# Performance work log

Hardware: AMD Instinct MI355X
Metric: run time of the kernel (lower is better)

The kernel has to match this reference:

```python
import jax, jax.numpy as jnp
import numpy as np

B, X_DIM, Z_DIM, K = 16384, 784, 64, 64
LOG2PI = 1.8378770664093453


def setup_inputs() -> dict:
    key = jax.random.key(0)
    ks = jax.random.split(key, 8)
    pi_raw = jax.random.uniform(ks[1], (B, K), dtype=jnp.float32) + 1e-3
    pi = pi_raw / jnp.sum(pi_raw, axis=1, keepdims=True)
    return {
        "x": jax.random.normal(ks[0], (B, X_DIM), dtype=jnp.float32),
        "pi": pi,
        "qz_mu": jax.random.normal(ks[2], (B, Z_DIM), dtype=jnp.float32),
        "qz_logsigma": 0.5 * jax.random.normal(ks[3], (B, Z_DIM), dtype=jnp.float32),
        "eps": jax.random.normal(ks[4], (B, Z_DIM), dtype=jnp.float32),
        "pz_y_mu": jax.random.normal(ks[5], (K, Z_DIM), dtype=jnp.float32),
        "pz_y_logsigma": jnp.zeros((K, Z_DIM), dtype=jnp.float32),  # log(init_sigma=1.0)
        "W_dec": jax.random.normal(ks[6], (Z_DIM, X_DIM), dtype=jnp.float32) / np.sqrt(Z_DIM),
        "b_dec": jnp.zeros((X_DIM,), dtype=jnp.float32),
    }


def reference(x, pi, qz_mu, qz_logsigma, eps, pz_y_mu, pz_y_logsigma, W_dec, b_dec):
    # GMMVAE.elbo with num_samples=1; rsample reparameterized with fixed eps.
    qs = jnp.exp(qz_logsigma)                      # [B, z]
    z = qz_mu + qs * eps                           # [B, z]

    # log p(x | z): unit-variance Gaussian likelihood with linear decoder
    mean = z @ W_dec + b_dec                       # [B, x]
    log_px_z = jnp.sum(-0.5 * (x - mean) ** 2 - 0.5 * LOG2PI)

    # py_z: vectorized over all k components (fuses the original Python loop)
    ps = jnp.exp(pz_y_logsigma)                    # [k, z]
    diff = z[:, None, :] - pz_y_mu[None, :, :]     # [B, k, z]
    comp_lp = jnp.sum(-0.5 * (diff / ps[None]) ** 2 - pz_y_logsigma[None] - 0.5 * LOG2PI, axis=-1)  # [B, k]
    log_pi = jnp.log(pi)
    pzy = comp_lp + log_pi                         # [B, k]
    log_py_z = pzy - jax.scipy.special.logsumexp(pzy, axis=1, keepdims=True)
    probs = jnp.exp(log_py_z)                      # [B, k]

    # kl_y = sum_b KL(Cat(py_z) || Cat(pi))
    kl_y = jnp.sum(probs * (log_py_z - log_pi))

    # kl_z = sum_b sum_k probs[b,k] * KL(N(qz_mu, qs) || N(mu_k, ps_k)).sum(z)
    mdiff = qz_mu[:, None, :] - pz_y_mu[None, :, :]  # [B, k, z]
    klz_bk = jnp.sum(
        pz_y_logsigma[None] - qz_logsigma[:, None, :]
        + (qs[:, None, :] ** 2 + mdiff ** 2) / (2.0 * ps[None] ** 2)
        - 0.5,
        axis=-1,
    )                                              # [B, k]
    kl_z = jnp.sum(probs * klz_bk)

    elbo = (log_px_z - kl_y - kl_z) / x.shape[0]
    return elbo
```

## Files before the change

### kernel.cpp

```cpp
#include <hip/hip_runtime.h>

#define NB 16384
#define XD 784
#define ZD 64
#define KK 64
#define LOG2PI_F 1.8378770664093453f
#define LDA 72

typedef __attribute__((ext_vector_type(8))) short short8;
typedef __attribute__((ext_vector_type(4))) float floatx4;


__device__ __forceinline__ float wave_sum(float x) {
    #pragma unroll
    for (int o = 32; o > 0; o >>= 1) x += __shfl_xor(x, o, 64);
    return x;
}

__device__ __forceinline__ unsigned short f2bf(float f) {
    unsigned u = __float_as_uint(f);
    unsigned r = (u + 0x7FFF + ((u >> 16) & 1)) >> 16;
    return (unsigned short)r;
}

__device__ __forceinline__ unsigned int pack2(float a, float b) {
    return (unsigned int)f2bf(a) | ((unsigned int)f2bf(b) << 16);
}

__global__ __launch_bounds__(256) void prep_kernel(
    const float* __restrict__ W, unsigned short* __restrict__ Wt)
{
    int idx = blockIdx.x * 256 + threadIdx.x;
    if (idx < ZD * XD) {
        int k = idx / XD;
        int n = idx - k * XD;
        Wt[n * ZD + k] = f2bf(W[idx]);
    }
}

__global__ __launch_bounds__(256) void mixture_mfma_kernel(
    const float* __restrict__ pi, const float* __restrict__ qmu,
    const float* __restrict__ qls, const float* __restrict__ eps,
    const float* __restrict__ pmu_g, const float* __restrict__ plog_g,
    float* __restrict__ kly_p, float* __restrict__ klz_p)
{
    __shared__ unsigned short Az2[64 * LDA];
    __shared__ unsigned short Azm[64 * LDA];
    __shared__ unsigned short Aq2[64 * LDA];
    __shared__ unsigned short Aqm[64 * LDA];
    __shared__ unsigned short Bi2[64 * LDA];
    __shared__ unsigned short Bm1[64 * LDA];
    __shared__ float Ck_s[KK], Sk_s[KK], Gk_s[KK], sq_s[64];
    __shared__ float r1[4], r2[4];

    const int tid  = threadIdx.x;
    const int row0 = blockIdx.x * 64;

    {
        const int r  = tid >> 2;
        const int q  = tid & 3;
        const int v0 = q * 16;
        const int gb = (row0 + r) * 64 + v0;
        float4 mu4[4], ls4[4], ep4[4];
        #pragma unroll
        for (int i = 0; i < 4; ++i) {
            mu4[i] = *(const float4*)&qmu[gb + 4 * i];
            ls4[i] = *(const float4*)&qls[gb + 4 * i];
            ep4[i] = *(const float4*)&eps[gb + 4 * i];
        }
        float sls = 0.f;
        unsigned int* pz2 = (unsigned int*)&Az2[r * LDA + v0];
        unsigned int* pzm = (unsigned int*)&Azm[r * LDA + v0];
        unsigned int* pq2 = (unsigned int*)&Aq2[r * LDA + v0];
        unsigned int* pqm = (unsigned int*)&Aqm[r * LDA + v0];
        #pragma unroll
        for (int i = 0; i < 4; ++i) {
            float m0[4] = {mu4[i].x, mu4[i].y, mu4[i].z, mu4[i].w};
            float l0[4] = {ls4[i].x, ls4[i].y, ls4[i].z, ls4[i].w};
            float e0[4] = {ep4[i].x, ep4[i].y, ep4[i].z, ep4[i].w};
            float z[4], q2[4];
            #pragma unroll
            for (int j = 0; j < 4; ++j) {
                float qs = __expf(l0[j]);
                z[j]  = fmaf(qs, e0[j], m0[j]);
                q2[j] = fmaf(m0[j], m0[j], qs * qs);
                sls += l0[j];
            }
            pz2[i * 2 + 0] = pack2(z[0] * z[0], z[1] * z[1]);
            pz2[i * 2 + 1] = pack2(z[2] * z[2], z[3] * z[3]);
            pzm[i * 2 + 0] = pack2(-2.f * z[0], -2.f * z[1]);
            pzm[i * 2 + 1] = pack2(-2.f * z[2], -2.f * z[3]);
            pq2[i * 2 + 0] = pack2(q2[0], q2[1]);
            pq2[i * 2 + 1] = pack2(q2[2], q2[3]);
            pqm[i * 2 + 0] = pack2(-2.f * m0[0], -2.f * m0[1]);
            pqm[i * 2 + 1] = pack2(-2.f * m0[2], -2.f * m0[3]);
        }
        sls += __shfl_xor(sls, 1, 64);
        sls += __shfl_xor(sls, 2, 64);
        if (q == 0) sq_s[r] = sls;
    }

    {
        const int k  = tid >> 2;
        const int q  = tid & 3;
        const int v0 = q * 16;
        const int gb = k * 64 + v0;
        float s = 0.f, g = 0.f;
        unsigned int* pi2 = (unsigned int*)&Bi2[k * LDA + v0];
        unsigned int* pm1 = (unsigned int*)&Bm1[k * LDA + v0];
        #pragma unroll
        for (int i = 0; i < 4; ++i) {
            float4 mu4 = *(const float4*)&pmu_g[gb + 4 * i];
            float4 lg4 = *(const float4*)&plog_g[gb + 4 * i];
            float m0[4] = {mu4.x, mu4.y, mu4.z, mu4.w};
            float l0[4] = {lg4.x, lg4.y, lg4.z, lg4.w};
            float i2v[4], m1v[4];
            #pragma unroll
            for (int j = 0; j < 4; ++j) {
                float i2 = 0.5f * __expf(-2.f * l0[j]);
                i2v[j] = i2;
                m1v[j] = m0[j] * i2;
                g = fmaf(m0[j] * m0[j], i2, g);
                s += l0[j];
            }
            pi2[i * 2 + 0] = pack2(i2v[0], i2v[1]);
            pi2[i * 2 + 1] = pack2(i2v[2], i2v[3]);
            pm1[i * 2 + 0] = pack2(m1v[0], m1v[1]);
            pm1[i * 2 + 1] = pack2(m1v[2], m1v[3]);
        }
        s += __shfl_xor(s, 1, 64);
        s += __shfl_xor(s, 2, 64);
        g += __shfl_xor(g, 1, 64);
        g += __shfl_xor(g, 2, 64);
        if (q == 0) {
            Sk_s[k] = s;
            Gk_s[k] = g;
            Ck_s[k] = -s - 32.0f * LOG2PI_F;
        }
    }
    __syncthreads();

    const int lane  = tid & 63;
    const int wid   = tid >> 6;
    const int mm    = lane & 15;
    const int quad  = lane >> 4;
    const int rbase = wid * 16;

    const short8 az2_0 = *(const short8*)&Az2[(rbase + mm) * LDA + quad * 8];
    const short8 az2_1 = *(const short8*)&Az2[(rbase + mm) * LDA + 32 + quad * 8];
    const short8 azm_0 = *(const short8*)&Azm[(rbase + mm) * LDA + quad * 8];
    const short8 azm_1 = *(const short8*)&Azm[(rbase + mm) * LDA + 32 + quad * 8];
    const short8 aq2_0 = *(const short8*)&Aq2[(rbase + mm) * LDA + quad * 8];
    const short8 aq2_1 = *(const short8*)&Aq2[(rbase + mm) * LDA + 32 + quad * 8];
    const short8 aqm_0 = *(const short8*)&Aqm[(rbase + mm) * LDA + quad * 8];
    const short8 aqm_1 = *(const short8*)&Aqm[(rbase + mm) * LDA + 32 + quad * 8];

    floatx4 acc_a[4], acc_c[4];
    #pragma unroll
    for (int t = 0; t < 4; ++t) {
        const int kr = t * 16 + mm;
        const short8 bi0 = *(const short8*)&Bi2[kr * LDA + quad * 8];
        const short8 bi1 = *(const short8*)&Bi2[kr * LDA + 32 + quad * 8];
        const short8 bm0 = *(const short8*)&Bm1[kr * LDA + quad * 8];
        const short8 bm1 = *(const short8*)&Bm1[kr * LDA + 32 + quad * 8];
        floatx4 ca = {0.f, 0.f, 0.f, 0.f};
        ca = __builtin_amdgcn_mfma_f32_16x16x32_bf16(az2_0, bi0, ca, 0, 0, 0);
        ca = __builtin_amdgcn_mfma_f32_16x16x32_bf16(az2_1, bi1, ca, 0, 0, 0);
        ca = __builtin_amdgcn_mfma_f32_16x16x32_bf16(azm_0, bm0, ca, 0, 0, 0);
        ca = __builtin_amdgcn_mfma_f32_16x16x32_bf16(azm_1, bm1, ca, 0, 0, 0);
        acc_a[t] = ca;
        floatx4 cc = {0.f, 0.f, 0.f, 0.f};
        cc = __builtin_amdgcn_mfma_f32_16x16x32_bf16(aq2_0, bi0, cc, 0, 0, 0);
        cc = __builtin_amdgcn_mfma_f32_16x16x32_bf16(aq2_1, bi1, cc, 0, 0, 0);
        cc = __builtin_amdgcn_mfma_f32_16x16x32_bf16(aqm_0, bm0, cc, 0, 0, 0);
        cc = __builtin_amdgcn_mfma_f32_16x16x32_bf16(aqm_1, bm1, cc, 0, 0, 0);
        acc_c[t] = cc;
    }

    float comp[4][4], pz[4][4];
    #pragma unroll
    for (int t = 0; t < 4; ++t) {
        const int k = t * 16 + mm;
        const float ck = Ck_s[k], gk = Gk_s[k];
        #pragma unroll
        for (int r = 0; r < 4; ++r) {
            const int gb = row0 + rbase + quad * 4 + r;
            comp[t][r] = ck - (acc_a[t][r] + gk);
            pz[t][r] = comp[t][r] + __logf(pi[gb * 64 + k]);
        }
    }

    float kly = 0.f, klz = 0.f;
    #pragma unroll
    for (int r = 0; r < 4; ++r) {
        float mx = fmaxf(fmaxf(pz[0][r], pz[1][r]), fmaxf(pz[2][r], pz[3][r]));
        #pragma unroll
        for (int o = 1; o <= 8; o <<= 1) mx = fmaxf(mx, __shfl_xor(mx, o, 64));
        float e[4];
        float s = 0.f;
        #pragma unroll
        for (int t = 0; t < 4; ++t) { e[t] = __expf(pz[t][r] - mx); s += e[t]; }
        #pragma unroll
        for (int o = 1; o <= 8; o <<= 1) s += __shfl_xor(s, o, 64);
        const float lse = mx + __logf(s);
        const float inv = __frcp_rn(s);
        const float sql = sq_s[rbase + quad * 4 + r];
        #pragma unroll
        for (int t = 0; t < 4; ++t) {
            const int k = t * 16 + mm;
            const float p = e[t] * inv;
            kly = fmaf(p, comp[t][r] - lse, kly);
            const float cv = acc_c[t][r] + Gk_s[k];
            klz = fmaf(p, Sk_s[k] - sql + cv - 32.0f, klz);
        }
    }

    kly = wave_sum(kly);
    klz = wave_sum(klz);
    if (lane == 0) { r1[wid] = kly; r2[wid] = klz; }
    __syncthreads();
    if (tid == 0) {
        kly_p[blockIdx.x] = r1[0] + r1[1] + r1[2] + r1[3];
        klz_p[blockIdx.x] = r2[0] + r2[1] + r2[2] + r2[3];
    }
}

__global__ __launch_bounds__(256) void decoder_mfma_kernel(
    const float* __restrict__ x, const float* __restrict__ qmu,
    const float* __restrict__ qls, const float* __restrict__ eps,
    const unsigned short* __restrict__ Wt, const float* __restrict__ bd,
    float* __restrict__ dec_p)
{
    __shared__ unsigned short zt[16 * 64];
    __shared__ float rs[4];
    const int tid  = threadIdx.x;
    const int row0 = blockIdx.x * 16;

    for (int i = tid; i < 16 * 64; i += 256) {
        int g = row0 * 64 + i;
        float z = fmaf(__expf(qls[g]), eps[g], qmu[g]);
        zt[i] = f2bf(z);
    }
    __syncthreads();

    const int lane = tid & 63;
    const int wid  = tid >> 6;
    const int m    = lane & 15;
    const int quad = lane >> 4;

    const short8 af0 = *(const short8*)&zt[m * 64 + quad * 8];
    const short8 af1 = *(const short8*)&zt[m * 64 + 32 + quad * 8];

    const int xrow = (row0 + quad * 4) * XD;

    float xa0, xa1, xa2, xa3, bb;
    short8 w0, w1;
    {
        const int col = wid * 16 + m;
        xa0 = x[xrow + 0 * XD + col];
        xa1 = x[xrow + 1 * XD + col];
        xa2 = x[xrow + 2 * XD + col];
        xa3 = x[xrow + 3 * XD + col];
        bb  = bd[col];
        w0  = *(const short8*)&Wt[col * 64 + quad * 8];
        w1  = *(const short8*)&Wt[col * 64 + 32 + quad * 8];
    }

    float accl = 0.f;
    #pragma unroll 1
    for (int t = wid; t < 49; t += 4) {
        const float cx0 = xa0, cx1 = xa1, cx2 = xa2, cx3 = xa3, cb = bb;
        const short8 cw0 = w0, cw1 = w1;
        const int tn = t + 4;
        if (tn < 49) {
            const int col = tn * 16 + m;
            xa0 = x[xrow + 0 * XD + col];
            xa1 = x[xrow + 1 * XD + col];
            xa2 = x[xrow + 2 * XD + col];
            xa3 = x[xrow + 3 * XD + col];
            bb  = bd[col];
            w0  = *(const short8*)&Wt[col * 64 + quad * 8];
            w1  = *(const short8*)&Wt[col * 64 + 32 + quad * 8];
        }
        floatx4 c = {0.f, 0.f, 0.f, 0.f};
        c = __builtin_amdgcn_mfma_f32_16x16x32_bf16(af0, cw0, c, 0, 0, 0);
        c = __builtin_amdgcn_mfma_f32_16x16x32_bf16(af1, cw1, c, 0, 0, 0);
        float d0 = cx0 - (c[0] + cb);
        float d1 = cx1 - (c[1] + cb);
        float d2 = cx2 - (c[2] + cb);
        float d3 = cx3 - (c[3] + cb);
        accl = fmaf(d0, d0, accl);
        accl = fmaf(d1, d1, accl);
        accl = fmaf(d2, d2, accl);
        accl = fmaf(d3, d3, accl);
    }

    float s = wave_sum(accl);
    if (lane == 0) rs[wid] = s;
    __syncthreads();
    if (tid == 0)
        dec_p[blockIdx.x] = -0.5f * (rs[0] + rs[1] + rs[2] + rs[3]);
}

__global__ __launch_bounds__(256) void finalize_kernel(
    const float* __restrict__ dec_p, const float* __restrict__ kly_p,
    const float* __restrict__ klz_p, float* __restrict__ out)
{
    __shared__ double s0[256], s1[256], s2[256];
    const int tid = threadIdx.x;
    double a0 = 0.0, a1 = 0.0, a2 = 0.0;
    for (int i = tid; i < 1024; i += 256) a0 += (double)dec_p[i];
    a1 = (double)kly_p[tid];
    a2 = (double)klz_p[tid];
    s0[tid] = a0; s1[tid] = a1; s2[tid] = a2;
    __syncthreads();
    #pragma unroll
    for (int off = 128; off > 0; off >>= 1) {
        if (tid < off) {
            s0[tid] += s0[tid + off];
            s1[tid] += s1[tid + off];
            s2[tid] += s2[tid + off];
        }
        __syncthreads();
    }
    if (tid == 0) {
        double lpx = s0[0] - 0.5 * 1.8378770664093453 * (double)NB * (double)XD;
        out[0] = (float)((lpx - s1[0] - s2[0]) / (double)NB);
    }
}

extern "C" void kernel_launch(void* const* d_in, const int* in_sizes, int n_in,
                              void* d_out, int out_size, void* d_ws, size_t ws_size,
                              hipStream_t stream) {
    const float* x    = (const float*)d_in[0];
    const float* pi   = (const float*)d_in[1];
    const float* qmu  = (const float*)d_in[2];
    const float* qls  = (const float*)d_in[3];
    const float* eps  = (const float*)d_in[4];
    const float* pmu  = (const float*)d_in[5];
    const float* plog = (const float*)d_in[6];
    const float* W    = (const float*)d_in[7];
    const float* bd   = (const float*)d_in[8];
    float* out = (float*)d_out;

    unsigned short* Wt = (unsigned short*)d_ws;
    float* fp    = (float*)((char*)d_ws + 100352);
    float* dec_p = fp;
    float* kly_p = fp + 1024;
    float* klz_p = fp + 1280;

    prep_kernel<<<(ZD * XD + 255) / 256, 256, 0, stream>>>(W, Wt);
    mixture_mfma_kernel<<<NB / 64, 256, 0, stream>>>(pi, qmu, qls, eps, pmu, plog, kly_p, klz_p);
    decoder_mfma_kernel<<<NB / 16, 256, 0, stream>>>(x, qmu, qls, eps, Wt, bd, dec_p);
    finalize_kernel<<<1, 256, 0, stream>>>(dec_p, kly_p, klz_p, out);
}
```

Baseline: 127.2 us.

## Fuse mixture and decoder kernels, precompute mixture params in prep kernel

Merges the mixture-KL kernel and the decoder kernel into a single kernel where each wave owns 16 rows and builds its bf16 MFMA operands directly in registers, with no shared-memory staging. The per-component terms (inverse variances, scaled means, Sk, Gk) move into an extra block of the prep kernel, so each block no longer recomputes them. This removes one launch, the repeated reads of qmu/qls/eps, and the block-level syncs. In exchange each wave walks all 49 decoder column tiles serially, so there are fewer blocks in flight (256 blocks of 4 waves) to hide the x-load latency, and register pressure goes up.

New measurement: 137.5 us. 1.08x slower.

```diff
diff --git a/kernel.cpp b/kernel.cpp
--- a/kernel.cpp
+++ b/kernel.cpp
@@ -5,7 +5,6 @@
 #define ZD 64
 #define KK 64
 #define LOG2PI_F 1.8378770664093453f
-#define LDA 72
 
 typedef __attribute__((ext_vector_type(8))) short short8;
 typedef __attribute__((ext_vector_type(4))) float floatx4;
@@ -27,166 +26,163 @@
     return (unsigned int)f2bf(a) | ((unsigned int)f2bf(b) << 16);
 }
 
+__device__ __forceinline__ short8 pack8(const float* v) {
+    short8 r;
+    unsigned int* p = (unsigned int*)&r;
+    p[0] = pack2(v[0], v[1]);
+    p[1] = pack2(v[2], v[3]);
+    p[2] = pack2(v[4], v[5]);
+    p[3] = pack2(v[6], v[7]);
+    return r;
+}
+
 __global__ __launch_bounds__(256) void prep_kernel(
-    const float* __restrict__ W, unsigned short* __restrict__ Wt)
+    const float* __restrict__ W, const float* __restrict__ pmu_g,
+    const float* __restrict__ plog_g, unsigned short* __restrict__ Wt,
+    unsigned short* __restrict__ Bi2, unsigned short* __restrict__ Bm1,
+    float* __restrict__ Sk, float* __restrict__ Gk)
 {
-    int idx = blockIdx.x * 256 + threadIdx.x;
-    if (idx < ZD * XD) {
+    const int tid = threadIdx.x;
+    if (blockIdx.x < 196) {
+        int idx = blockIdx.x * 256 + tid;
         int k = idx / XD;
         int n = idx - k * XD;
         Wt[n * ZD + k] = f2bf(W[idx]);
-    }
-}
-
-__global__ __launch_bounds__(256) void mixture_mfma_kernel(
-    const float* __restrict__ pi, const float* __restrict__ qmu,
-    const float* __restrict__ qls, const float* __restrict__ eps,
-    const float* __restrict__ pmu_g, const float* __restrict__ plog_g,
-    float* __restrict__ kly_p, float* __restrict__ klz_p)
+        return;
+    }
+    const int k  = tid >> 2;
+    const int q  = tid & 3;
+    const int v0 = q * 16;
+    float s = 0.f, g = 0.f;
+    unsigned int* pi2 = (unsigned int*)&Bi2[k * 64 + v0];
+    unsigned int* pm1 = (unsigned int*)&Bm1[k * 64 + v0];
+    #pragma unroll
+    for (int i = 0; i < 4; ++i) {
+        float4 mu4 = *(const float4*)&pmu_g[k * 64 + v0 + 4 * i];
+        float4 lg4 = *(const float4*)&plog_g[k * 64 + v0 + 4 * i];
+        float m0[4] = {mu4.x, mu4.y, mu4.z, mu4.w};
+        float l0[4] = {lg4.x, lg4.y, lg4.z, lg4.w};
+        float i2v[4], m1v[4];
+        #pragma unroll
+        for (int j = 0; j < 4; ++j) {
+            float i2 = 0.5f * __expf(-2.f * l0[j]);
+            i2v[j] = i2;
+            m1v[j] = m0[j] * i2;
+            g = fmaf(m0[j] * m0[j], i2, g);
+            s += l0[j];
+        }
+        pi2[i * 2 + 0] = pack2(i2v[0], i2v[1]);
+        pi2[i * 2 + 1] = pack2(i2v[2], i2v[3]);
+        pm1[i * 2 + 0] = pack2(m1v[0], m1v[1]);
+        pm1[i * 2 + 1] = pack2(m1v[2], m1v[3]);
+    }
+    s += __shfl_xor(s, 1, 64);
+    s += __shfl_xor(s, 2, 64);
+    g += __shfl_xor(g, 1, 64);
+    g += __shfl_xor(g, 2, 64);
+    if (q == 0) { Sk[k] = s; Gk[k] = g; }
+}
+
+__global__ __launch_bounds__(256) void fused_kernel(
+    const float* __restrict__ x, const float* __restrict__ pi,
+    const float* __restrict__ qmu, const float* __restrict__ qls,
+    const float* __restrict__ eps,
+    const unsigned short* __restrict__ Bi2, const unsigned short* __restrict__ Bm1,
+    const float* __restrict__ Sk, const float* __restrict__ Gk,
+    const unsigned short* __restrict__ Wt, const float* __restrict__ bd,
+    float* __restrict__ dec_p, float* __restrict__ kly_p, float* __restrict__ klz_p)
 {
-    __shared__ unsigned short Az2[64 * LDA];
-    __shared__ unsigned short Azm[64 * LDA];
-    __shared__ unsigned short Aq2[64 * LDA];
-    __shared__ unsigned short Aqm[64 * LDA];
-    __shared__ unsigned short Bi2[64 * LDA];
-    __shared__ unsigned short Bm1[64 * LDA];
-    __shared__ float Ck_s[KK], Sk_s[KK], Gk_s[KK], sq_s[64];
-    __shared__ float r1[4], r2[4];
-
-    const int tid  = threadIdx.x;
-    const int row0 = blockIdx.x * 64;
-
-    {
-        const int r  = tid >> 2;
-        const int q  = tid & 3;
-        const int v0 = q * 16;
-        const int gb = (row0 + r) * 64 + v0;
-        float4 mu4[4], ls4[4], ep4[4];
-        #pragma unroll
-        for (int i = 0; i < 4; ++i) {
-            mu4[i] = *(const float4*)&qmu[gb + 4 * i];
-            ls4[i] = *(const float4*)&qls[gb + 4 * i];
-            ep4[i] = *(const float4*)&eps[gb + 4 * i];
-        }
-        float sls = 0.f;
-        unsigned int* pz2 = (unsigned int*)&Az2[r * LDA + v0];
-        unsigned int* pzm = (unsigned int*)&Azm[r * LDA + v0];
-        unsigned int* pq2 = (unsigned int*)&Aq2[r * LDA + v0];
-        unsigned int* pqm = (unsigned int*)&Aqm[r * LDA + v0];
-        #pragma unroll
-        for (int i = 0; i < 4; ++i) {
-            float m0[4] = {mu4[i].x, mu4[i].y, mu4[i].z, mu4[i].w};
-            float l0[4] = {ls4[i].x, ls4[i].y, ls4[i].z, ls4[i].w};
-            float e0[4] = {ep4[i].x, ep4[i].y, ep4[i].z, ep4[i].w};
-            float z[4], q2[4];
-            #pragma unroll
-            for (int j = 0; j < 4; ++j) {
-                float qs = __expf(l0[j]);
-                z[j]  = fmaf(qs, e0[j], m0[j]);
-                q2[j] = fmaf(m0[j], m0[j], qs * qs);
-                sls += l0[j];
-            }
-            pz2[i * 2 + 0] = pack2(z[0] * z[0], z[1] * z[1]);
-            pz2[i * 2 + 1] = pack2(z[2] * z[2], z[3] * z[3]);
-            pzm[i * 2 + 0] = pack2(-2.f * z[0], -2.f * z[1]);
-            pzm[i * 2 + 1] = pack2(-2.f * z[2], -2.f * z[3]);
-            pq2[i * 2 + 0] = pack2(q2[0], q2[1]);
-            pq2[i * 2 + 1] = pack2(q2[2], q2[3]);
-            pqm[i * 2 + 0] = pack2(-2.f * m0[0], -2.f * m0[1]);
-            pqm[i * 2 + 1] = pack2(-2.f * m0[2], -2.f * m0[3]);
-        }
-        sls += __shfl_xor(sls, 1, 64);
-        sls += __shfl_xor(sls, 2, 64);
-        if (q == 0) sq_s[r] = sls;
-    }
-
-    {
-        const int k  = tid >> 2;
-        const int q  = tid & 3;
-        const int v0 = q * 16;
-        const int gb = k * 64 + v0;
-        float s = 0.f, g = 0.f;
-        unsigned int* pi2 = (unsigned int*)&Bi2[k * LDA + v0];
-        unsigned int* pm1 = (unsigned int*)&Bm1[k * LDA + v0];
-        #pragma unroll
-        for (int i = 0; i < 4; ++i) {
-            float4 mu4 = *(const float4*)&pmu_g[gb + 4 * i];
-            float4 lg4 = *(const float4*)&plog_g[gb + 4 * i];
-            float m0[4] = {mu4.x, mu4.y, mu4.z, mu4.w};
-            float l0[4] = {lg4.x, lg4.y, lg4.z, lg4.w};
-            float i2v[4], m1v[4];
-            #pragma unroll
-            for (int j = 0; j < 4; ++j) {
-                float i2 = 0.5f * __expf(-2.f * l0[j]);
-                i2v[j] = i2;
-                m1v[j] = m0[j] * i2;
-                g = fmaf(m0[j] * m0[j], i2, g);
-                s += l0[j];
-            }
-            pi2[i * 2 + 0] = pack2(i2v[0], i2v[1]);
-            pi2[i * 2 + 1] = pack2(i2v[2], i2v[3]);
-            pm1[i * 2 + 0] = pack2(m1v[0], m1v[1]);
-            pm1[i * 2 + 1] = pack2(m1v[2], m1v[3]);
-        }
-        s += __shfl_xor(s, 1, 64);
-        s += __shfl_xor(s, 2, 64);
-        g += __shfl_xor(g, 1, 64);
-        g += __shfl_xor(g, 2, 64);
-        if (q == 0) {
-            Sk_s[k] = s;
-            Gk_s[k] = g;
-            Ck_s[k] = -s - 32.0f * LOG2PI_F;
-        }
-    }
-    __syncthreads();
-
+    const int tid   = threadIdx.x;
     const int lane  = tid & 63;
     const int wid   = tid >> 6;
     const int mm    = lane & 15;
     const int quad  = lane >> 4;
-    const int rbase = wid * 16;
-
-    const short8 az2_0 = *(const short8*)&Az2[(rbase + mm) * LDA + quad * 8];
-    const short8 az2_1 = *(const short8*)&Az2[(rbase + mm) * LDA + 32 + quad * 8];
-    const short8 azm_0 = *(const short8*)&Azm[(rbase + mm) * LDA + quad * 8];
-    const short8 azm_1 = *(const short8*)&Azm[(rbase + mm) * LDA + 32 + quad * 8];
-    const short8 aq2_0 = *(const short8*)&Aq2[(rbase + mm) * LDA + quad * 8];
-    const short8 aq2_1 = *(const short8*)&Aq2[(rbase + mm) * LDA + 32 + quad * 8];
-    const short8 aqm_0 = *(const short8*)&Aqm[(rbase + mm) * LDA + quad * 8];
-    const short8 aqm_1 = *(const short8*)&Aqm[(rbase + mm) * LDA + 32 + quad * 8];
+    const int row0  = blockIdx.x * 64;
+    const int crow0 = row0 + wid * 16;
+    const int arow  = crow0 + mm;
+    const int v0    = quad * 8;
+    const int v1    = 32 + quad * 8;
+
+    float mu[16], ls[16], ep[16];
+    *(float4*)&mu[0]  = *(const float4*)&qmu[arow * 64 + v0];
+    *(float4*)&mu[4]  = *(const float4*)&qmu[arow * 64 + v0 + 4];
+    *(float4*)&mu[8]  = *(const float4*)&qmu[arow * 64 + v1];
+    *(float4*)&mu[12] = *(const float4*)&qmu[arow * 64 + v1 + 4];
+    *(float4*)&ls[0]  = *(const float4*)&qls[arow * 64 + v0];
+    *(float4*)&ls[4]  = *(const float4*)&qls[arow * 64 + v0 + 4];
+    *(float4*)&ls[8]  = *(const float4*)&qls[arow * 64 + v1];
+    *(float4*)&ls[12] = *(const float4*)&qls[arow * 64 + v1 + 4];
+    *(float4*)&ep[0]  = *(const float4*)&eps[arow * 64 + v0];
+    *(float4*)&ep[4]  = *(const float4*)&eps[arow * 64 + v0 + 4];
+    *(float4*)&ep[8]  = *(const float4*)&eps[arow * 64 + v1];
+    *(float4*)&ep[12] = *(const float4*)&eps[arow * 64 + v1 + 4];
+
+    float zf[16], zz[16], zm[16], q2[16], qm[16];
+    float sls = 0.f;
+    #pragma unroll
+    for (int j = 0; j < 16; ++j) {
+        float qs = __expf(ls[j]);
+        float z  = fmaf(qs, ep[j], mu[j]);
+        zf[j] = z;
+        zz[j] = z * z;
+        zm[j] = -2.f * z;
+        q2[j] = fmaf(mu[j], mu[j], qs * qs);
+        qm[j] = -2.f * mu[j];
+        sls += ls[j];
+    }
+    sls += __shfl_xor(sls, 16, 64);
+    sls += __shfl_xor(sls, 32, 64);
+
+    const short8 az2_0 = pack8(&zz[0]), az2_1 = pack8(&zz[8]);
+    const short8 azm_0 = pack8(&zm[0]), azm_1 = pack8(&zm[8]);
+    const short8 aq2_0 = pack8(&q2[0]), aq2_1 = pack8(&q2[8]);
+    const short8 aqm_0 = pack8(&qm[0]), aqm_1 = pack8(&qm[8]);
+    const short8 af0   = pack8(&zf[0]), af1   = pack8(&zf[8]);
+
+    short8 bi[4][2], bm[4][2];
+    float skv[4], gkv[4];
+    #pragma unroll
+    for (int t = 0; t < 4; ++t) {
+        const int kc = t * 16 + mm;
+        bi[t][0] = *(const short8*)&Bi2[kc * 64 + v0];
+        bi[t][1] = *(const short8*)&Bi2[kc * 64 + v1];
+        bm[t][0] = *(const short8*)&Bm1[kc * 64 + v0];
+        bm[t][1] = *(const short8*)&Bm1[kc * 64 + v1];
+        skv[t] = Sk[kc];
+        gkv[t] = Gk[kc];
+    }
+    float pv[4][4];
+    #pragma unroll
+    for (int t = 0; t < 4; ++t)
+        #pragma unroll
+        for (int r = 0; r < 4; ++r)
+            pv[t][r] = pi[(crow0 + quad * 4 + r) * 64 + t * 16 + mm];
 
     floatx4 acc_a[4], acc_c[4];
     #pragma unroll
     for (int t = 0; t < 4; ++t) {
-        const int kr = t * 16 + mm;
-        const short8 bi0 = *(const short8*)&Bi2[kr * LDA + quad * 8];
-        const short8 bi1 = *(const short8*)&Bi2[kr * LDA + 32 + quad * 8];
-        const short8 bm0 = *(const short8*)&Bm1[kr * LDA + quad * 8];
-        const short8 bm1 = *(const short8*)&Bm1[kr * LDA + 32 + quad * 8];
         floatx4 ca = {0.f, 0.f, 0.f, 0.f};
-        ca = __builtin_amdgcn_mfma_f32_16x16x32_bf16(az2_0, bi0, ca, 0, 0, 0);
-        ca = __builtin_amdgcn_mfma_f32_16x16x32_bf16(az2_1, bi1, ca, 0, 0, 0);
-        ca = __builtin_amdgcn_mfma_f32_16x16x32_bf16(azm_0, bm0, ca, 0, 0, 0);
-        ca = __builtin_amdgcn_mfma_f32_16x16x32_bf16(azm_1, bm1, ca, 0, 0, 0);
+        ca = __builtin_amdgcn_mfma_f32_16x16x32_bf16(az2_0, bi[t][0], ca, 0, 0, 0);
+        ca = __builtin_amdgcn_mfma_f32_16x16x32_bf16(az2_1, bi[t][1], ca, 0, 0, 0);
+        ca = __builtin_amdgcn_mfma_f32_16x16x32_bf16(azm_0, bm[t][0], ca, 0, 0, 0);
+        ca = __builtin_amdgcn_mfma_f32_16x16x32_bf16(azm_1, bm[t][1], ca, 0, 0, 0);
         acc_a[t] = ca;
         floatx4 cc = {0.f, 0.f, 0.f, 0.f};
-        cc = __builtin_amdgcn_mfma_f32_16x16x32_bf16(aq2_0, bi0, cc, 0, 0, 0);
-        cc = __builtin_amdgcn_mfma_f32_16x16x32_bf16(aq2_1, bi1, cc, 0, 0, 0);
-        cc = __builtin_amdgcn_mfma_f32_16x16x32_bf16(aqm_0, bm0, cc, 0, 0, 0);
-        cc = __builtin_amdgcn_mfma_f32_16x16x32_bf16(aqm_1, bm1, cc, 0, 0, 0);
+        cc = __builtin_amdgcn_mfma_f32_16x16x32_bf16(aq2_0, bi[t][0], cc, 0, 0, 0);
+        cc = __builtin_amdgcn_mfma_f32_16x16x32_bf16(aq2_1, bi[t][1], cc, 0, 0, 0);
+        cc = __builtin_amdgcn_mfma_f32_16x16x32_bf16(aqm_0, bm[t][0], cc, 0, 0, 0);
+        cc = __builtin_amdgcn_mfma_f32_16x16x32_bf16(aqm_1, bm[t][1], cc, 0, 0, 0);
         acc_c[t] = cc;
     }
 
     float comp[4][4], pz[4][4];
     #pragma unroll
     for (int t = 0; t < 4; ++t) {
-        const int k = t * 16 + mm;
-        const float ck = Ck_s[k], gk = Gk_s[k];
+        const float ck = -skv[t] - 32.0f * LOG2PI_F;
         #pragma unroll
         for (int r = 0; r < 4; ++r) {
-            const int gb = row0 + rbase + quad * 4 + r;
-            comp[t][r] = ck - (acc_a[t][r] + gk);
-            pz[t][r] = comp[t][r] + __logf(pi[gb * 64 + k]);
+            comp[t][r] = ck - (acc_a[t][r] + gkv[t]);
+            pz[t][r] = comp[t][r] + __logf(pv[t][r]);
         }
     }
 
@@ -204,83 +200,50 @@
         for (int o = 1; o <= 8; o <<= 1) s += __shfl_xor(s, o, 64);
         const float lse = mx + __logf(s);
         const float inv = __frcp_rn(s);
-        const float sql = sq_s[rbase + quad * 4 + r];
+        const float sqr = __shfl(sls, quad * 4 + r, 64);
         #pragma unroll
         for (int t = 0; t < 4; ++t) {
-            const int k = t * 16 + mm;
             const float p = e[t] * inv;
             kly = fmaf(p, comp[t][r] - lse, kly);
-            const float cv = acc_c[t][r] + Gk_s[k];
-            klz = fmaf(p, Sk_s[k] - sql + cv - 32.0f, klz);
+            klz = fmaf(p, skv[t] - sqr + acc_c[t][r] + gkv[t] - 32.0f, klz);
         }
     }
 
     kly = wave_sum(kly);
     klz = wave_sum(klz);
-    if (lane == 0) { r1[wid] = kly; r2[wid] = klz; }
-    __syncthreads();
-    if (tid == 0) {
-        kly_p[blockIdx.x] = r1[0] + r1[1] + r1[2] + r1[3];
-        klz_p[blockIdx.x] = r2[0] + r2[1] + r2[2] + r2[3];
-    }
-}
-
-__global__ __launch_bounds__(256) void decoder_mfma_kernel(
-    const float* __restrict__ x, const float* __restrict__ qmu,
-    const float* __restrict__ qls, const float* __restrict__ eps,
-    const unsigned short* __restrict__ Wt, const float* __restrict__ bd,
-    float* __restrict__ dec_p)
-{
-    __shared__ unsigned short zt[16 * 64];
-    __shared__ float rs[4];
-    const int tid  = threadIdx.x;
-    const int row0 = blockIdx.x * 16;
-
-    for (int i = tid; i < 16 * 64; i += 256) {
-        int g = row0 * 64 + i;
-        float z = fmaf(__expf(qls[g]), eps[g], qmu[g]);
-        zt[i] = f2bf(z);
-    }
-    __syncthreads();
-
-    const int lane = tid & 63;
-    const int wid  = tid >> 6;
-    const int m    = lane & 15;
-    const int quad = lane >> 4;
-
-    const short8 af0 = *(const short8*)&zt[m * 64 + quad * 8];
-    const short8 af1 = *(const short8*)&zt[m * 64 + 32 + quad * 8];
-
-    const int xrow = (row0 + quad * 4) * XD;
-
+    if (lane == 0) {
+        kly_p[blockIdx.x * 4 + wid] = kly;
+        klz_p[blockIdx.x * 4 + wid] = klz;
+    }
+
+    const int xrow = (crow0 + quad * 4) * XD;
     float xa0, xa1, xa2, xa3, bb;
     short8 w0, w1;
     {
-        const int col = wid * 16 + m;
+        const int col = mm;
         xa0 = x[xrow + 0 * XD + col];
         xa1 = x[xrow + 1 * XD + col];
         xa2 = x[xrow + 2 * XD + col];
         xa3 = x[xrow + 3 * XD + col];
         bb  = bd[col];
-        w0  = *(const short8*)&Wt[col * 64 + quad * 8];
-        w1  = *(const short8*)&Wt[col * 64 + 32 + quad * 8];
+        w0  = *(const short8*)&Wt[col * 64 + v0];
+        w1  = *(const short8*)&Wt[col * 64 + v1];
     }
 
     float accl = 0.f;
     #pragma unroll 1
-    for (int t = wid; t < 49; t += 4) {
+    for (int t = 0; t < 49; ++t) {
         const float cx0 = xa0, cx1 = xa1, cx2 = xa2, cx3 = xa3, cb = bb;
         const short8 cw0 = w0, cw1 = w1;
-        const int tn = t + 4;
-        if (tn < 49) {
-            const int col = tn * 16 + m;
+        if (t + 1 < 49) {
+            const int col = (t + 1) * 16 + mm;
             xa0 = x[xrow + 0 * XD + col];
             xa1 = x[xrow + 1 * XD + col];
             xa2 = x[xrow + 2 * XD + col];
             xa3 = x[xrow + 3 * XD + col];
             bb  = bd[col];
-            w0  = *(const short8*)&Wt[col * 64 + quad * 8];
-            w1  = *(const short8*)&Wt[col * 64 + 32 + quad * 8];
+            w0  = *(const short8*)&Wt[col * 64 + v0];
+            w1  = *(const short8*)&Wt[col * 64 + v1];
         }
         floatx4 c = {0.f, 0.f, 0.f, 0.f};
         c = __builtin_amdgcn_mfma_f32_16x16x32_bf16(af0, cw0, c, 0, 0, 0);
@@ -295,11 +258,8 @@
         accl = fmaf(d3, d3, accl);
     }
 
-    float s = wave_sum(accl);
-    if (lane == 0) rs[wid] = s;
-    __syncthreads();
-    if (tid == 0)
-        dec_p[blockIdx.x] = -0.5f * (rs[0] + rs[1] + rs[2] + rs[3]);
+    accl = wave_sum(accl);
+    if (lane == 0) dec_p[blockIdx.x * 4 + wid] = -0.5f * accl;
 }
 
 __global__ __launch_bounds__(256) void finalize_kernel(
@@ -309,9 +269,12 @@
     __shared__ double s0[256], s1[256], s2[256];
     const int tid = threadIdx.x;
     double a0 = 0.0, a1 = 0.0, a2 = 0.0;
-    for (int i = tid; i < 1024; i += 256) a0 += (double)dec_p[i];
-    a1 = (double)kly_p[tid];
-    a2 = (double)klz_p[tid];
+    #pragma unroll
+    for (int i = 0; i < 4; ++i) {
+        a0 += (double)dec_p[tid + 256 * i];
+        a1 += (double)kly_p[tid + 256 * i];
+        a2 += (double)klz_p[tid + 256 * i];
+    }
     s0[tid] = a0; s1[tid] = a1; s2[tid] = a2;
     __syncthreads();
     #pragma unroll
@@ -343,14 +306,19 @@
     const float* bd   = (const float*)d_in[8];
     float* out = (float*)d_out;
 
-    unsigned short* Wt = (unsigned short*)d_ws;
-    float* fp    = (float*)((char*)d_ws + 100352);
-    float* dec_p = fp;
-    float* kly_p = fp + 1024;
-    float* klz_p = fp + 1280;
-
-    prep_kernel<<<(ZD * XD + 255) / 256, 256, 0, stream>>>(W, Wt);
-    mixture_mfma_kernel<<<NB / 64, 256, 0, stream>>>(pi, qmu, qls, eps, pmu, plog, kly_p, klz_p);
-    decoder_mfma_kernel<<<NB / 16, 256, 0, stream>>>(x, qmu, qls, eps, Wt, bd, dec_p);
+    char* ws = (char*)d_ws;
+    unsigned short* Wt  = (unsigned short*)(ws);
+    unsigned short* Bi2 = (unsigned short*)(ws + 100352);
+    unsigned short* Bm1 = (unsigned short*)(ws + 108544);
+    float* Sk    = (float*)(ws + 116736);
+    float* Gk    = (float*)(ws + 116992);
+    float* dec_p = (float*)(ws + 117248);
+    float* kly_p = (float*)(ws + 121344);
+    float* klz_p = (float*)(ws + 125440);
+
+    prep_kernel<<<197, 256, 0, stream>>>(W, pmu, plog, Wt, Bi2, Bm1, Sk, Gk);
+    fused_kernel<<<NB / 64, 256, 0, stream>>>(x, pi, qmu, qls, eps,
+                                              Bi2, Bm1, Sk, Gk, Wt, bd,
+                                              dec_p, kly_p, klz_p);
     finalize_kernel<<<1, 256, 0, stream>>>(dec_p, kly_p, klz_p, out);
 }
```
